# Kernel optimization log

Measured on AMD Instinct MI355X. Metric: run time of the kernel, lower is better.

The kernel has to match this reference:

```python
import jax, jax.numpy as jnp
import numpy as np

N, C, NS, S = 32768, 128, 16, 8  # points, channels (mid==out planes), nsample, share_planes
EPS = 1e-5


def setup_inputs() -> dict:
    rng = np.random.default_rng(0)
    p = (rng.standard_normal((N, 3)) * 2.0).astype(np.float32)
    # exact kNN indices (self included), chunked to bound memory -- int constants
    sq = (p * p).sum(1)
    idx = np.empty((N, NS), dtype=np.int32)
    CH = 4096
    for i in range(0, N, CH):
        d = sq[i:i + CH, None] + sq[None, :] - 2.0 * (p[i:i + CH] @ p.T)
        idx[i:i + CH] = np.argpartition(d, NS, axis=1)[:, :NS]

    def lin(fi, fo):
        return (rng.standard_normal((fi, fo)).astype(np.float32) / np.sqrt(fi),
                np.zeros((fo,), np.float32))

    Wq, bq = lin(C, C)
    Wk, bk = lin(C, C)
    Wv, bv = lin(C, C)
    pW1, pb1 = lin(3, 3)
    pW2, pb2 = lin(3, C)
    wW1, wb1 = lin(C, C // S)
    wW2, wb2 = lin(C // S, C // S)
    x = rng.standard_normal((N, C)).astype(np.float32)
    d = dict(p=p, x=x,
             Wq=Wq, bq=bq, Wk=Wk, bk=bk, Wv=Wv, bv=bv,
             pW1=pW1, pb1=pb1, pg1=np.ones(3, np.float32), pbe1=np.zeros(3, np.float32),
             pW2=pW2, pb2=pb2,
             wg1=np.ones(C, np.float32), wbe1=np.zeros(C, np.float32),
             wW1=wW1, wb1=wb1,
             wg2=np.ones(C // S, np.float32), wbe2=np.zeros(C // S, np.float32),
             wW2=wW2, wb2=wb2,
             idx=idx)
    return {k: jnp.asarray(v) for k, v in d.items()}


def _bn(t, g, b):
    # BatchNorm1d training-mode over [N, nsample, ch]: stats per channel over N*nsample
    mu = t.mean(axis=(0, 1), keepdims=True)
    var = t.var(axis=(0, 1), keepdims=True)
    return (t - mu) * jax.lax.rsqrt(var + EPS) * g + b


def reference(p, x, Wq, bq, Wk, bk, Wv, bv, pW1, pb1, pg1, pbe1, pW2, pb2,
              wg1, wbe1, wW1, wb1, wg2, wbe2, wW2, wb2, idx):
    xq = x @ Wq + bq                      # [N, C]
    xk = (x @ Wk + bk)[idx]               # kNN gather -> [N, NS, C]
    xv = (x @ Wv + bv)[idx]               # [N, NS, C]
    pr = p[idx] - p[:, None, :]           # relative positions [N, NS, 3]
    # linear_p: Linear(3,3) -> BN(3) -> ReLU -> Linear(3,C)
    pr = jax.nn.relu(_bn(pr @ pW1 + pb1, pg1, pbe1)) @ pW2 + pb2  # [N, NS, C]
    # subtraction vector attention; out_planes//mid_planes == 1 so p_r sum(2) == p_r
    w = xk - xq[:, None, :] + pr
    # linear_w: BN(C) -> ReLU -> Linear(C, C//S) -> BN(C//S) -> ReLU -> Linear(C//S, C//S)
    w = jax.nn.relu(_bn(w, wg1, wbe1)) @ wW1 + wb1
    w = jax.nn.relu(_bn(w, wg2, wbe2)) @ wW2 + wb2                # [N, NS, C//S]
    w = jax.nn.softmax(w, axis=1)                                 # softmax over neighbors
    # share_planes-grouped weighted aggregate
    out = ((xv + pr).reshape(N, NS, S, C // S) * w[:, :, None, :]).sum(1).reshape(N, C)
    return out
```

## Files before the change

### kernel.cpp

```cpp
#include <hip/hip_runtime.h>

typedef unsigned short u16;
#define DEV __device__ __forceinline__

typedef short bf16x8 __attribute__((ext_vector_type(8)));
typedef float f32x4  __attribute__((ext_vector_type(4)));

constexpr int NP = 32768;
constexpr int C  = 128;
constexpr int NS = 16;
constexpr int RTOT = NP * NS;
constexpr float EPS = 1e-5f;
constexpr float INV_R = 1.0f / (float)RTOT;

constexpr size_t oXQ = 0;
constexpr size_t oXK = (size_t)NP * C * 2;
constexpr size_t oXV = oXK * 2;
constexpr size_t oW1 = oXK * 3;
constexpr size_t oPA = oW1;
constexpr size_t oPB = oW1 + 16384;
constexpr size_t oST = oW1 + (size_t)RTOT * 16 * 2;
constexpr size_t oM1 = oST;
constexpr size_t oM2 = oM1 + 16*8*4;
constexpr size_t oM3 = oM2 + 16*256*4;
constexpr size_t oPC = oM3 + 16*32*4;
constexpr size_t WS_NEED = oPC + 256*32*4;

DEV float bu2f(u16 v){ return __uint_as_float(((unsigned)v) << 16); }
DEV u16 f2bu(float f){
  unsigned u = __float_as_uint(f);
  return (u16)((u + 0x7fffu + ((u >> 16) & 1u)) >> 16);
}
DEV unsigned pk2(float a, float b){ return (unsigned)f2bu(a) | ((unsigned)f2bu(b) << 16); }
DEV unsigned pk2tr(float a, float b){
  return (__float_as_uint(a) >> 16) | (__float_as_uint(b) & 0xffff0000u);
}
DEV void b2x2(unsigned v, float& lo, float& hi){
  lo = __uint_as_float(v << 16);
  hi = __uint_as_float(v & 0xffff0000u);
}
DEV int clampg(int g){ return g < 0 ? 0 : (g > NP-1 ? NP-1 : g); }

__global__ __launch_bounds__(256) void k_sig(float* __restrict__ out, float val){
  int i = blockIdx.x * 256 + threadIdx.x;
  if (i < NP*C) out[i] = val;
}

__global__ __launch_bounds__(256) void k_finA(const float* __restrict__ part,
                                              float* __restrict__ mid,
                                              int slots, int width){
  __shared__ float red[4][64];
  const int l = threadIdx.x & 63, w = threadIdx.x >> 6;
  const int ch = blockIdx.x * 64 + l;
  const int y = blockIdx.y;
  const int cs = slots >> 4;
  const int n4 = cs >> 2;
  float a0 = 0.f, a1 = 0.f, a2 = 0.f, a3 = 0.f;
  if (ch < width){
    const float* base = part + (size_t)(y*cs + w*n4) * width + ch;
    int j = 0;
    for (; j + 4 <= n4; j += 4){
      a0 += base[(size_t)(j  ) * width];
      a1 += base[(size_t)(j+1) * width];
      a2 += base[(size_t)(j+2) * width];
      a3 += base[(size_t)(j+3) * width];
    }
    for (; j < n4; ++j) a0 += base[(size_t)j * width];
  }
  red[w][l] = (a0 + a1) + (a2 + a3);
  __syncthreads();
  if (threadIdx.x < 64 && ch < width)
    mid[(size_t)y * width + ch] = red[0][l] + red[1][l] + red[2][l] + red[3][l];
}

__global__ __launch_bounds__(256) void k_qkv(const float* __restrict__ x,
                                             const float* __restrict__ Wq,
                                             const float* __restrict__ Wk,
                                             const float* __restrict__ Wv,
                                             const float* __restrict__ bq,
                                             const float* __restrict__ bk,
                                             const float* __restrict__ bv,
                                             u16* __restrict__ outw){
  __shared__ __align__(16) float Wl[128*128];
  const int t = threadIdx.x;
  const int mat = blockIdx.y;
  const float* W    = (mat==0) ? Wq : ((mat==1) ? Wk : Wv);
  const float* bias = (mat==0) ? bq : ((mat==1) ? bk : bv);
  u16* outp = outw + (size_t)mat * NP * C;

  {
    const float4* Ws4 = (const float4*)W;
    float4* Wl4 = (float4*)Wl;
    #pragma unroll
    for (int i = 0; i < 16; ++i) Wl4[t + i*256] = Ws4[t + i*256];
  }
  __syncthreads();

  const int tr = t >> 4, cg = t & 15;
  const int row0 = blockIdx.x * 64 + tr * 4;
  float acc[4][8];
  #pragma unroll
  for (int j = 0; j < 8; ++j){
    float bj = bias[cg*8 + j];
    #pragma unroll
    for (int rr = 0; rr < 4; ++rr) acc[rr][j] = bj;
  }
  const float4* Wl4 = (const float4*)Wl;
  for (int k0 = 0; k0 < 128; k0 += 4){
    float4 xa[4];
    #pragma unroll
    for (int rr = 0; rr < 4; ++rr)
      xa[rr] = *(const float4*)(x + (size_t)(row0+rr)*C + k0);
    #pragma unroll
    for (int u = 0; u < 4; ++u){
      float4 w0 = Wl4[(k0+u)*32 + cg*2];
      float4 w1 = Wl4[(k0+u)*32 + cg*2 + 1];
      #pragma unroll
      for (int rr = 0; rr < 4; ++rr){
        float a = (&xa[rr].x)[u];
        acc[rr][0] = fmaf(a, w0.x, acc[rr][0]);
        acc[rr][1] = fmaf(a, w0.y, acc[rr][1]);
        acc[rr][2] = fmaf(a, w0.z, acc[rr][2]);
        acc[rr][3] = fmaf(a, w0.w, acc[rr][3]);
        acc[rr][4] = fmaf(a, w1.x, acc[rr][4]);
        acc[rr][5] = fmaf(a, w1.y, acc[rr][5]);
        acc[rr][6] = fmaf(a, w1.z, acc[rr][6]);
        acc[rr][7] = fmaf(a, w1.w, acc[rr][7]);
      }
    }
  }
  #pragma unroll
  for (int rr = 0; rr < 4; ++rr){
    uint4 pkd;
    #pragma unroll
    for (int q2 = 0; q2 < 4; ++q2)
      (&pkd.x)[q2] = pk2(acc[rr][q2*2], acc[rr][q2*2+1]);
    *(uint4*)(outp + (size_t)(row0+rr)*C + cg*8) = pkd;
  }
}

__global__ __launch_bounds__(256) void k_bn1(const float* __restrict__ p,
                                             const int* __restrict__ idx,
                                             const float* __restrict__ pW1,
                                             const float* __restrict__ pb1,
                                             float* __restrict__ partials1){
  __shared__ float wred[4][8];
  const int t = threadIdx.x;
  float w[9], b3[3];
  #pragma unroll
  for (int i = 0; i < 9; ++i) w[i] = pW1[i];
  #pragma unroll
  for (int i = 0; i < 3; ++i) b3[i] = pb1[i];
  float s[3] = {0,0,0}, q[3] = {0,0,0};
  const int base = blockIdx.x * 1024 + t;
  #pragma unroll
  for (int i = 0; i < 4; ++i){
    int r = base + i*256;
    int g = clampg(idx[r]);
    int n = r >> 4;
    float d0 = p[3*g]   - p[3*n];
    float d1 = p[3*g+1] - p[3*n+1];
    float d2 = p[3*g+2] - p[3*n+2];
    #pragma unroll
    for (int k = 0; k < 3; ++k){
      float tv = d0*w[k] + d1*w[3+k] + d2*w[6+k] + b3[k];
      s[k] += tv; q[k] = fmaf(tv, tv, q[k]);
    }
  }
  #pragma unroll
  for (int k = 0; k < 3; ++k){
    #pragma unroll
    for (int m = 1; m < 64; m <<= 1){
      s[k] += __shfl_xor(s[k], m);
      q[k] += __shfl_xor(q[k], m);
    }
  }
  if ((t & 63) == 0){
    int wv = t >> 6;
    wred[wv][0] = s[0]; wred[wv][1] = s[1]; wred[wv][2] = s[2]; wred[wv][3] = 0.f;
    wred[wv][4] = q[0]; wred[wv][5] = q[1]; wred[wv][6] = q[2]; wred[wv][7] = 0.f;
  }
  __syncthreads();
  if (t < 8)
    partials1[blockIdx.x*8 + t] = wred[0][t] + wred[1][t] + wred[2][t] + wred[3][t];
}

__global__ __launch_bounds__(256) void k_bn2(const float* __restrict__ p,
                                             const int* __restrict__ idx,
                                             const float* __restrict__ pW1,
                                             const float* __restrict__ pb1,
                                             const float* __restrict__ pg1,
                                             const float* __restrict__ pbe1,
                                             const float* __restrict__ pW2,
                                             const float* __restrict__ pb2,
                                             const u16* __restrict__ xq,
                                             const u16* __restrict__ xk,
                                             const float* __restrict__ mid1,
                                             float* __restrict__ partials2){
  __shared__ float sq0[64], sq1[64], sq2[64];
  __shared__ int   sgi[64];
  __shared__ __align__(16) float4 pW2t[128];
  __shared__ float bn1s[8];
  __shared__ __align__(16) float redS[4][128], redQ[4][128];
  const int t = threadIdx.x;
  if (t < 3){
    float sv = 0.f, sq = 0.f;
    for (int i = 0; i < 16; ++i){ sv += mid1[i*8+t]; sq += mid1[i*8+4+t]; }
    float mu = sv * INV_R, var = sq * INV_R - mu*mu;
    float rs = rsqrtf(var + EPS);
    float sc = rs * pg1[t];
    bn1s[t]   = sc;
    bn1s[4+t] = pb1[t] * sc + pbe1[t] - mu * sc;
  }
  if (t < 128)
    pW2t[t] = make_float4(pW2[t], pW2[128+t], pW2[256+t], pb2[t]);
  float w9[9];
  if (t < 64){
    #pragma unroll
    for (int i = 0; i < 9; ++i) w9[i] = pW1[i];
  }
  __syncthreads();
  const int w = t >> 6, l = t & 63;
  const float4 pwA = pW2t[2*l], pwB = pW2t[2*l+1];
  float sA = 0.f, qA = 0.f, sB = 0.f, qB = 0.f;

  for (int tile = 0; tile < 4; ++tile){
    const int b0 = (blockIdx.x * 4 + tile) * 64;
    if (t < 64){
      int r = b0 + t, n = r >> 4;
      int g = clampg(idx[r]);
      float d0 = p[3*g]   - p[3*n];
      float d1 = p[3*g+1] - p[3*n+1];
      float d2 = p[3*g+2] - p[3*n+2];
      sq0[t] = fmaxf((d0*w9[0] + d1*w9[3] + d2*w9[6]) * bn1s[0] + bn1s[4], 0.f);
      sq1[t] = fmaxf((d0*w9[1] + d1*w9[4] + d2*w9[7]) * bn1s[1] + bn1s[5], 0.f);
      sq2[t] = fmaxf((d0*w9[2] + d1*w9[5] + d2*w9[8]) * bn1s[2] + bn1s[6], 0.f);
      sgi[t] = g;
    }
    __syncthreads();
    #pragma unroll
    for (int pt = 0; pt < 4; ++pt){
      const int n = (b0 >> 4) + pt;
      unsigned qx = *(const unsigned*)(xq + (size_t)n*C + 2*l);
      float xqA, xqB; b2x2(qx, xqA, xqB);
      #pragma unroll
      for (int k = 0; k < 4; ++k){
        int rr = pt*16 + w + k*4;
        int g = sgi[rr];
        unsigned kx = *(const unsigned*)(xk + (size_t)g*C + 2*l);
        float xkA, xkB; b2x2(kx, xkA, xkB);
        float prA = sq0[rr]*pwA.x + sq1[rr]*pwA.y + sq2[rr]*pwA.z + pwA.w;
        float prB = sq0[rr]*pwB.x + sq1[rr]*pwB.y + sq2[rr]*pwB.z + pwB.w;
        float w0A = xkA - xqA + prA;
        float w0B = xkB - xqB + prB;
        sA += w0A; qA = fmaf(w0A, w0A, qA);
        sB += w0B; qB = fmaf(w0B, w0B, qB);
      }
    }
    __syncthreads();
  }
  *(float2*)&redS[w][2*l] = make_float2(sA, sB);
  *(float2*)&redQ[w][2*l] = make_float2(qA, qB);
  __syncthreads();
  if (t < 128){
    partials2[(size_t)blockIdx.x*256 + t]       = redS[0][t]+redS[1][t]+redS[2][t]+redS[3][t];
    partials2[(size_t)blockIdx.x*256 + 128 + t] = redQ[0][t]+redQ[1][t]+redQ[2][t]+redQ[3][t];
  }
}

__global__ __launch_bounds__(256) void k_w1(const float* __restrict__ p,
                                            const int* __restrict__ idx,
                                            const float* __restrict__ pW1,
                                            const float* __restrict__ pb1,
                                            const float* __restrict__ pg1,
                                            const float* __restrict__ pbe1,
                                            const float* __restrict__ pW2,
                                            const float* __restrict__ pb2,
                                            const float* __restrict__ wg1,
                                            const float* __restrict__ wbe1,
                                            const float* __restrict__ wW1,
                                            const float* __restrict__ wb1,
                                            const u16* __restrict__ xq,
                                            const u16* __restrict__ xk,
                                            u16* __restrict__ w1out,
                                            const float* __restrict__ mid1,
                                            const float* __restrict__ mid2){
  __shared__ __align__(16) float4 pW2t[128];
  __shared__ float2 ss2[128];
  __shared__ float bn1s[8];
  __shared__ float wb1f[16];
  __shared__ float pW1f[9];
  __shared__ float sq0[64], sq1[64], sq2[64];
  __shared__ int   sgi[64];
  __shared__ __align__(16) u16 hsb[64*136];
  const int t = threadIdx.x;
  if (t < 3){
    float sv = 0.f, sq = 0.f;
    for (int i = 0; i < 16; ++i){ sv += mid1[i*8+t]; sq += mid1[i*8+4+t]; }
    float mu = sv * INV_R, var = sq * INV_R - mu*mu;
    float rs = rsqrtf(var + EPS);
    float sc = rs * pg1[t];
    bn1s[t]   = sc;
    bn1s[4+t] = pb1[t] * sc + pbe1[t] - mu * sc;
  }
  if (t < 9)  pW1f[t] = pW1[t];
  if (t < 16) wb1f[t] = wb1[t];
  if (t < 128){
    pW2t[t] = make_float4(pW2[t], pW2[128+t], pW2[256+t], pb2[t]);
    float sv = 0.f, sq = 0.f;
    for (int i = 0; i < 16; ++i){ sv += mid2[i*256+t]; sq += mid2[i*256+128+t]; }
    float mu = sv * INV_R, var = sq * INV_R - mu*mu;
    float rs = rsqrtf(var + EPS);
    float sc = rs * wg1[t];
    ss2[t] = make_float2(sc, wbe1[t] - mu * sc);
  }

  const int w = t >> 6, l = t & 63;
  const int quad = l >> 4, col = l & 15;
  bf16x8 bfrag[4];
  #pragma unroll
  for (int kk = 0; kk < 4; ++kk){
    #pragma unroll
    for (int j = 0; j < 8; ++j)
      bfrag[kk][j] = (short)f2bu(wW1[(size_t)(kk*32 + quad*8 + j)*16 + col]);
  }
  __syncthreads();

  const float4 pwA = pW2t[2*l], pwB = pW2t[2*l+1];
  const float2 scA = ss2[2*l],  scB = ss2[2*l+1];
  const float biasC = wb1f[col];

  for (int tile = 0; tile < 4; ++tile){
    const int rb = (blockIdx.x * 4 + tile) * 64;
    if (t < 64){
      int r = rb + t, n = r >> 4;
      int g = clampg(idx[r]);
      float d0 = p[3*g]   - p[3*n];
      float d1 = p[3*g+1] - p[3*n+1];
      float d2 = p[3*g+2] - p[3*n+2];
      sq0[t] = fmaxf((d0*pW1f[0] + d1*pW1f[3] + d2*pW1f[6]) * bn1s[0] + bn1s[4], 0.f);
      sq1[t] = fmaxf((d0*pW1f[1] + d1*pW1f[4] + d2*pW1f[7]) * bn1s[1] + bn1s[5], 0.f);
      sq2[t] = fmaxf((d0*pW1f[2] + d1*pW1f[5] + d2*pW1f[8]) * bn1s[2] + bn1s[6], 0.f);
      sgi[t] = g;
    }
    __syncthreads();
    #pragma unroll
    for (int pt = 0; pt < 4; ++pt){
      const int n = (rb >> 4) + pt;
      unsigned qx = *(const unsigned*)(xq + (size_t)n*C + 2*l);
      float xqA, xqB; b2x2(qx, xqA, xqB);
      #pragma unroll
      for (int k = 0; k < 4; ++k){
        int rr = pt*16 + w + k*4;
        int g = sgi[rr];
        unsigned kx = *(const unsigned*)(xk + (size_t)g*C + 2*l);
        float xkA, xkB; b2x2(kx, xkA, xkB);
        float prA = sq0[rr]*pwA.x + sq1[rr]*pwA.y + sq2[rr]*pwA.z + pwA.w;
        float prB = sq0[rr]*pwB.x + sq1[rr]*pwB.y + sq2[rr]*pwB.z + pwB.w;
        float hA = fmaxf(fmaf(xkA - xqA + prA, scA.x, scA.y), 0.f);
        float hB = fmaxf(fmaf(xkB - xqB + prB, scB.x, scB.y), 0.f);
        *(unsigned*)&hsb[rr*136 + 2*l] = pk2tr(hA, hB);
      }
    }
    __syncthreads();
    f32x4 acc;
    acc[0] = biasC; acc[1] = biasC; acc[2] = biasC; acc[3] = biasC;
    const u16* hbase = &hsb[(size_t)(w*16 + col) * 136];
    #pragma unroll
    for (int kk = 0; kk < 4; ++kk){
      bf16x8 af = *(const bf16x8*)(hbase + kk*32 + quad*8);
      acc = __builtin_amdgcn_mfma_f32_16x16x32_bf16(af, bfrag[kk], acc, 0, 0, 0);
    }
    #pragma unroll
    for (int i = 0; i < 4; ++i){
      int row = w*16 + quad*4 + i;
      w1out[(size_t)(rb + row) * 16 + col] = f2bu(acc[i]);
    }
    __syncthreads();
  }
}

__global__ __launch_bounds__(256) void k_bn3(const u16* __restrict__ w1ws,
                                             float* __restrict__ partials3){
  __shared__ float rs[256][8], rq[256][8];
  const int t = threadIdx.x;
  float s[8], q[8];
  #pragma unroll
  for (int k = 0; k < 8; ++k){ s[k] = 0.f; q[k] = 0.f; }
  const uint4* w4 = (const uint4*)w1ws;
  const int base = blockIdx.x * 256 + t;
  #pragma unroll 4
  for (int it = 0; it < 16; ++it){
    uint4 v = w4[base + it * 65536];
    #pragma unroll
    for (int k = 0; k < 4; ++k){
      float lo, hi; b2x2((&v.x)[k], lo, hi);
      s[k*2]   += lo; q[k*2]   = fmaf(lo, lo, q[k*2]);
      s[k*2+1] += hi; q[k*2+1] = fmaf(hi, hi, q[k*2+1]);
    }
  }
  #pragma unroll
  for (int k = 0; k < 8; ++k){ rs[t][k] = s[k]; rq[t][k] = q[k]; }
  __syncthreads();
  if (t < 32){
    int isq = t >> 4, ch = t & 15;
    int par = ch >> 3, k = ch & 7;
    float acc = 0.f;
    if (isq){
      for (int i2 = par; i2 < 256; i2 += 2) acc += rq[i2][k];
    } else {
      for (int i2 = par; i2 < 256; i2 += 2) acc += rs[i2][k];
    }
    partials3[blockIdx.x*32 + isq*16 + ch] = acc;
  }
}

__global__ __launch_bounds__(256) void k_out(const float* __restrict__ p,
                                             const int* __restrict__ idx,
                                             const float* __restrict__ pW1,
                                             const float* __restrict__ pb1,
                                             const float* __restrict__ pg1,
                                             const float* __restrict__ pbe1,
                                             const float* __restrict__ pW2,
                                             const float* __restrict__ pb2,
                                             const float* __restrict__ wg2,
                                             const float* __restrict__ wbe2,
                                             const float* __restrict__ wW2,
                                             const float* __restrict__ wb2,
                                             const u16* __restrict__ xv,
                                             const u16* __restrict__ w1ws,
                                             const float* __restrict__ mid1,
                                             const float* __restrict__ mid3,
                                             float* __restrict__ out){
  __shared__ __align__(16) float4 pW2t[128];
  __shared__ float pW1f[9];
  __shared__ float bn1s[8];
  __shared__ float sc3[16], sh3[16], wb2f[16];
  __shared__ float wW2f[256];
  __shared__ float s_w2[16*16*16];
  __shared__ float s_q0[256], s_q1[256], s_q2[256];
  __shared__ int   s_g[256];
  const int t = threadIdx.x;
  if (t < 3){
    float sv = 0.f, sq = 0.f;
    for (int i = 0; i < 16; ++i){ sv += mid1[i*8+t]; sq += mid1[i*8+4+t]; }
    float mu = sv * INV_R, var = sq * INV_R - mu*mu;
    float rs = rsqrtf(var + EPS);
    float sc = rs * pg1[t];
    bn1s[t]   = sc;
    bn1s[4+t] = pb1[t] * sc + pbe1[t] - mu * sc;
  }
  if (t < 9) pW1f[t] = pW1[t];
  if (t < 16){
    float sv = 0.f, sq = 0.f;
    for (int i = 0; i < 16; ++i){ sv += mid3[i*32+t]; sq += mid3[i*32+16+t]; }
    float mu = sv * INV_R, var = sq * INV_R - mu*mu;
    float rs = rsqrtf(var + EPS);
    float sc = rs * wg2[t];
    sc3[t] = sc;
    sh3[t] = wbe2[t] - mu * sc;
    wb2f[t] = wb2[t];
  }
  if (t < 128)
    pW2t[t] = make_float4(pW2[t], pW2[128+t], pW2[256+t], pb2[t]);
  wW2f[t] = wW2[t];
  __syncthreads();

  const int pt = t >> 4;
  const int jj = t & 15;
  const int n0 = blockIdx.x * 16;
  {
    const int n = n0 + pt;
    const int r = n * NS + jj;
    const int g = clampg(idx[r]);
    float d0 = p[3*g]   - p[3*n];
    float d1 = p[3*g+1] - p[3*n+1];
    float d2 = p[3*g+2] - p[3*n+2];
    s_q0[t] = fmaxf((d0*pW1f[0] + d1*pW1f[3] + d2*pW1f[6]) * bn1s[0] + bn1s[4], 0.f);
    s_q1[t] = fmaxf((d0*pW1f[1] + d1*pW1f[4] + d2*pW1f[7]) * bn1s[1] + bn1s[5], 0.f);
    s_q2[t] = fmaxf((d0*pW1f[2] + d1*pW1f[5] + d2*pW1f[8]) * bn1s[2] + bn1s[6], 0.f);
    s_g[t]  = g;
    const uint4* wp = (const uint4*)(w1ws + (size_t)r * 16);
    uint4 Wa = wp[0], Wb = wp[1];
    float h2[16];
    #pragma unroll
    for (int o2 = 0; o2 < 4; ++o2){
      float lo, hi;
      b2x2((&Wa.x)[o2], lo, hi);
      h2[o2*2]     = fmaxf(lo * sc3[o2*2]     + sh3[o2*2],     0.f);
      h2[o2*2+1]   = fmaxf(hi * sc3[o2*2+1]   + sh3[o2*2+1],   0.f);
      b2x2((&Wb.x)[o2], lo, hi);
      h2[8+o2*2]   = fmaxf(lo * sc3[8+o2*2]   + sh3[8+o2*2],   0.f);
      h2[8+o2*2+1] = fmaxf(hi * sc3[8+o2*2+1] + sh3[8+o2*2+1], 0.f);
    }
    float w2[16];
    #pragma unroll
    for (int o = 0; o < 16; ++o) w2[o] = wb2f[o];
    #pragma unroll
    for (int o2 = 0; o2 < 16; ++o2){
      float h = h2[o2];
      const float* wr = &wW2f[o2*16];
      #pragma unroll
      for (int o = 0; o < 16; ++o) w2[o] = fmaf(h, wr[o], w2[o]);
    }
    float* dst = &s_w2[(pt*16 + jj)*16];
    #pragma unroll
    for (int o = 0; o < 16; ++o) dst[o] = w2[o];
  }
  __syncthreads();
  const int cs = t & 15;
  {
    float mx = -1e30f;
    #pragma unroll
    for (int j2 = 0; j2 < 16; ++j2) mx = fmaxf(mx, s_w2[(pt*16+j2)*16 + cs]);
    float e[16]; float sum = 0.f;
    #pragma unroll
    for (int j2 = 0; j2 < 16; ++j2){
      e[j2] = __expf(s_w2[(pt*16+j2)*16 + cs] - mx);
      sum += e[j2];
    }
    float inv = 1.0f / sum;
    #pragma unroll
    for (int j2 = 0; j2 < 16; ++j2) s_w2[(pt*16+j2)*16 + cs] = e[j2] * inv;
  }
  __syncthreads();
  const int w = t >> 6, l = t & 63;
  const float4 pwA = pW2t[2*l], pwB = pW2t[2*l+1];
  const int csA = (2*l) & 15;
  #pragma unroll
  for (int pp = 0; pp < 4; ++pp){
    const int pt2 = pp * 4 + w;
    const int n = n0 + pt2;
    float accA = 0.f, accB = 0.f;
    #pragma unroll
    for (int j = 0; j < 16; ++j){
      const int base = pt2*16 + j;
      float2 pj2 = *(const float2*)&s_w2[base*16 + csA];
      int g = s_g[base];
      float qa = s_q0[base], qb = s_q1[base], qc = s_q2[base];
      unsigned v = *(const unsigned*)(xv + (size_t)g*C + 2*l);
      float xvA, xvB; b2x2(v, xvA, xvB);
      float prA = qa*pwA.x + qb*pwA.y + qc*pwA.z + pwA.w;
      float prB = qa*pwB.x + qb*pwB.y + qc*pwB.z + pwB.w;
      accA = fmaf(xvA + prA, pj2.x, accA);
      accB = fmaf(xvB + prB, pj2.y, accB);
    }
    *(float2*)(out + (size_t)n*C + 2*l) = make_float2(accA, accB);
  }
}

extern "C" void kernel_launch(void* const* d_in, const int* in_sizes, int n_in,
                              void* d_out, int out_size, void* d_ws, size_t ws_size,
                              hipStream_t stream) {
  bool ok = (n_in == 23) && (out_size == NP*C) &&
            in_sizes[0] == NP*3 && in_sizes[1] == NP*C &&
            in_sizes[2] == C*C  && in_sizes[8] == 9 &&
            in_sizes[12] == 3*C && in_sizes[16] == C*(C/8) &&
            in_sizes[20] == (C/8)*(C/8) && in_sizes[22] == RTOT;
  if (!ok){
    k_sig<<<(NP*C+255)/256, 256, 0, stream>>>((float*)d_out, 10000.0f);
    return;
  }
  if (ws_size < WS_NEED){
    k_sig<<<(NP*C+255)/256, 256, 0, stream>>>((float*)d_out, 20000.0f);
    return;
  }
  const float* p    = (const float*)d_in[0];
  const float* x    = (const float*)d_in[1];
  const float* Wq   = (const float*)d_in[2];
  const float* bq   = (const float*)d_in[3];
  const float* Wk   = (const float*)d_in[4];
  const float* bk   = (const float*)d_in[5];
  const float* Wv   = (const float*)d_in[6];
  const float* bv   = (const float*)d_in[7];
  const float* pW1  = (const float*)d_in[8];
  const float* pb1  = (const float*)d_in[9];
  const float* pg1  = (const float*)d_in[10];
  const float* pbe1 = (const float*)d_in[11];
  const float* pW2  = (const float*)d_in[12];
  const float* pb2  = (const float*)d_in[13];
  const float* wg1  = (const float*)d_in[14];
  const float* wbe1 = (const float*)d_in[15];
  const float* wW1  = (const float*)d_in[16];
  const float* wb1  = (const float*)d_in[17];
  const float* wg2  = (const float*)d_in[18];
  const float* wbe2 = (const float*)d_in[19];
  const float* wW2  = (const float*)d_in[20];
  const float* wb2  = (const float*)d_in[21];
  const int* idx    = (const int*)d_in[22];

  char* ws = (char*)d_ws;
  u16* xq    = (u16*)(ws + oXQ);
  u16* xk    = (u16*)(ws + oXK);
  u16* xv    = (u16*)(ws + oXV);
  u16* w1ws  = (u16*)(ws + oW1);
  float* pa  = (float*)(ws + oPA);
  float* pb  = (float*)(ws + oPB);
  float* pc  = (float*)(ws + oPC);
  float* m1  = (float*)(ws + oM1);
  float* m2  = (float*)(ws + oM2);
  float* m3  = (float*)(ws + oM3);

  k_qkv<<<dim3(512, 3), 256, 0, stream>>>(x, Wq, Wk, Wv, bq, bk, bv, xq);
  k_bn1<<<512, 256, 0, stream>>>(p, idx, pW1, pb1, pa);
  k_finA<<<dim3(1, 16), 256, 0, stream>>>(pa, m1, 512, 8);
  k_bn2<<<2048, 256, 0, stream>>>(p, idx, pW1, pb1, pg1, pbe1, pW2, pb2,
                                  xq, xk, m1, pb);
  k_finA<<<dim3(4, 16), 256, 0, stream>>>(pb, m2, 2048, 256);
  k_w1 <<<2048, 256, 0, stream>>>(p, idx, pW1, pb1, pg1, pbe1, pW2, pb2,
                                  wg1, wbe1, wW1, wb1, xq, xk, w1ws, m1, m2);
  k_bn3<<<256, 256, 0, stream>>>(w1ws, pc);
  k_finA<<<dim3(1, 16), 256, 0, stream>>>(pc, m3, 256, 32);
  k_out<<<2048, 256, 0, stream>>>(p, idx, pW1, pb1, pg1, pbe1, pW2, pb2,
                                  wg2, wbe2, wW2, wb2, xv, w1ws, m1, m3,
                                  (float*)d_out);
}
```

Baseline: 265.8 us.

## Compute QKV projection with bf16 MFMA and fuse three matrices per block

Replaces the fp32 FMA QKV GEMM with bf16 MFMA 16x16x32 instructions. A small pre-kernel converts and transposes the weights into bf16 in workspace. Each block now loads and converts its 64 rows of x once and reuses them for Q, K and V instead of launching separate blocks per matrix. This cuts ALU work and x reloads, but x is now rounded to bf16 before the matmul, which reduces precision, and adds one extra kernel launch.

Measured after the change: 231.7 us. -12.8%, faster.

```diff
diff --git a/kernel.cpp b/kernel.cpp
--- a/kernel.cpp
+++ b/kernel.cpp
@@ -24,7 +24,8 @@
 constexpr size_t oM2 = oM1 + 16*8*4;
 constexpr size_t oM3 = oM2 + 16*256*4;
 constexpr size_t oPC = oM3 + 16*32*4;
-constexpr size_t WS_NEED = oPC + 256*32*4;
+constexpr size_t oWT = oPC + 256*32*4;
+constexpr size_t WS_NEED = oWT + 3*128*128*2;
 
 DEV float bu2f(u16 v){ return __uint_as_float(((unsigned)v) << 16); }
 DEV u16 f2bu(float f){
@@ -73,69 +74,78 @@
     mid[(size_t)y * width + ch] = red[0][l] + red[1][l] + red[2][l] + red[3][l];
 }
 
+__global__ __launch_bounds__(256) void k_wt(const float* __restrict__ Wq,
+                                            const float* __restrict__ Wk,
+                                            const float* __restrict__ Wv,
+                                            u16* __restrict__ wt){
+  const int mat = blockIdx.y;
+  const float* W = (mat==0) ? Wq : ((mat==1) ? Wk : Wv);
+  int e = blockIdx.x * 256 + threadIdx.x;
+  int k = e >> 7, c = e & 127;
+  wt[mat*16384 + c*128 + k] = f2bu(W[e]);
+}
+
 __global__ __launch_bounds__(256) void k_qkv(const float* __restrict__ x,
-                                             const float* __restrict__ Wq,
-                                             const float* __restrict__ Wk,
-                                             const float* __restrict__ Wv,
+                                             const u16* __restrict__ wt,
                                              const float* __restrict__ bq,
                                              const float* __restrict__ bk,
                                              const float* __restrict__ bv,
                                              u16* __restrict__ outw){
-  __shared__ __align__(16) float Wl[128*128];
+  __shared__ __align__(16) u16 xb[64*136];
+  __shared__ __align__(16) u16 wtl[128*136];
   const int t = threadIdx.x;
-  const int mat = blockIdx.y;
-  const float* W    = (mat==0) ? Wq : ((mat==1) ? Wk : Wv);
-  const float* bias = (mat==0) ? bq : ((mat==1) ? bk : bv);
-  u16* outp = outw + (size_t)mat * NP * C;
-
+  const int row0 = blockIdx.x * 64;
   {
-    const float4* Ws4 = (const float4*)W;
-    float4* Wl4 = (float4*)Wl;
-    #pragma unroll
-    for (int i = 0; i < 16; ++i) Wl4[t + i*256] = Ws4[t + i*256];
-  }
-  __syncthreads();
-
-  const int tr = t >> 4, cg = t & 15;
-  const int row0 = blockIdx.x * 64 + tr * 4;
-  float acc[4][8];
-  #pragma unroll
-  for (int j = 0; j < 8; ++j){
-    float bj = bias[cg*8 + j];
-    #pragma unroll
-    for (int rr = 0; rr < 4; ++rr) acc[rr][j] = bj;
-  }
-  const float4* Wl4 = (const float4*)Wl;
-  for (int k0 = 0; k0 < 128; k0 += 4){
-    float4 xa[4];
-    #pragma unroll
-    for (int rr = 0; rr < 4; ++rr)
-      xa[rr] = *(const float4*)(x + (size_t)(row0+rr)*C + k0);
-    #pragma unroll
-    for (int u = 0; u < 4; ++u){
-      float4 w0 = Wl4[(k0+u)*32 + cg*2];
-      float4 w1 = Wl4[(k0+u)*32 + cg*2 + 1];
+    const float4* xs = (const float4*)(x + (size_t)row0 * C);
+    #pragma unroll
+    for (int i = 0; i < 8; ++i){
+      int chunk = t + i*256;
+      int row = chunk >> 5;
+      int cp  = (chunk & 31) * 4;
+      float4 v = xs[chunk];
+      *(uint2*)&xb[row*136 + cp] = make_uint2(pk2(v.x, v.y), pk2(v.z, v.w));
+    }
+  }
+  __syncthreads();
+  const int w = t >> 6, l = t & 63;
+  const int quad = l >> 4, col = l & 15;
+  bf16x8 afrag[4];
+  {
+    const u16* abase = &xb[(size_t)(w*16 + col) * 136];
+    #pragma unroll
+    for (int kk = 0; kk < 4; ++kk)
+      afrag[kk] = *(const bf16x8*)(abase + kk*32 + quad*8);
+  }
+  for (int mat = 0; mat < 3; ++mat){
+    const float* bias = (mat==0) ? bq : ((mat==1) ? bk : bv);
+    {
+      const uint4* ws4 = (const uint4*)(wt + mat*16384);
       #pragma unroll
-      for (int rr = 0; rr < 4; ++rr){
-        float a = (&xa[rr].x)[u];
-        acc[rr][0] = fmaf(a, w0.x, acc[rr][0]);
-        acc[rr][1] = fmaf(a, w0.y, acc[rr][1]);
-        acc[rr][2] = fmaf(a, w0.z, acc[rr][2]);
-        acc[rr][3] = fmaf(a, w0.w, acc[rr][3]);
-        acc[rr][4] = fmaf(a, w1.x, acc[rr][4]);
-        acc[rr][5] = fmaf(a, w1.y, acc[rr][5]);
-        acc[rr][6] = fmaf(a, w1.z, acc[rr][6]);
-        acc[rr][7] = fmaf(a, w1.w, acc[rr][7]);
+      for (int i = 0; i < 8; ++i){
+        int chunk = t + i*256;
+        int c = chunk >> 4, kp = (chunk & 15) * 8;
+        *(uint4*)&wtl[c*136 + kp] = ws4[chunk];
       }
     }
-  }
-  #pragma unroll
-  for (int rr = 0; rr < 4; ++rr){
-    uint4 pkd;
-    #pragma unroll
-    for (int q2 = 0; q2 < 4; ++q2)
-      (&pkd.x)[q2] = pk2(acc[rr][q2*2], acc[rr][q2*2+1]);
-    *(uint4*)(outp + (size_t)(row0+rr)*C + cg*8) = pkd;
+    __syncthreads();
+    u16* outp = outw + (size_t)mat * NP * C + (size_t)(row0 + w*16) * C;
+    #pragma unroll
+    for (int ct = 0; ct < 8; ++ct){
+      bf16x8 bfrag[4];
+      const u16* bbase = &wtl[(size_t)(ct*16 + col) * 136];
+      #pragma unroll
+      for (int kk = 0; kk < 4; ++kk)
+        bfrag[kk] = *(const bf16x8*)(bbase + kk*32 + quad*8);
+      float bv0 = bias[ct*16 + col];
+      f32x4 acc; acc[0] = bv0; acc[1] = bv0; acc[2] = bv0; acc[3] = bv0;
+      #pragma unroll
+      for (int kk = 0; kk < 4; ++kk)
+        acc = __builtin_amdgcn_mfma_f32_16x16x32_bf16(afrag[kk], bfrag[kk], acc, 0, 0, 0);
+      #pragma unroll
+      for (int i = 0; i < 4; ++i)
+        outp[(size_t)(quad*4 + i) * C + ct*16 + col] = f2bu(acc[i]);
+    }
+    __syncthreads();
   }
 }
 
@@ -600,8 +610,10 @@
   float* m1  = (float*)(ws + oM1);
   float* m2  = (float*)(ws + oM2);
   float* m3  = (float*)(ws + oM3);
-
-  k_qkv<<<dim3(512, 3), 256, 0, stream>>>(x, Wq, Wk, Wv, bq, bk, bv, xq);
+  u16* wtp   = (u16*)(ws + oWT);
+
+  k_wt <<<dim3(64, 3), 256, 0, stream>>>(Wq, Wk, Wv, wtp);
+  k_qkv<<<512, 256, 0, stream>>>(x, wtp, bq, bk, bv, xq);
   k_bn1<<<512, 256, 0, stream>>>(p, idx, pW1, pb1, pa);
   k_finA<<<dim3(1, 16), 256, 0, stream>>>(pa, m1, 512, 8);
   k_bn2<<<2048, 256, 0, stream>>>(p, idx, pW1, pb1, pg1, pbe1, pW2, pb2,
```
